# Kernel tuning notes

Measured on AMD Instinct MI355X. Metric: run time of the kernel, lower is better.

Reference implementation:

```python
import jax, jax.numpy as jnp
import numpy as np

HS = 512; L = 4; T = 128; M = 2048; FF = 2048; NH = 4; DH = HS // NH
STDV = 1.0 / float(np.sqrt(HS))


def setup_inputs() -> dict:
    key = jax.random.key(0)
    ks = iter(jax.random.split(key, 32))

    def u(shape):
        return jax.random.uniform(next(ks), shape, jnp.float32, -STDV, STDV)

    return {
        "x": jax.random.normal(next(ks), (1, T, HS), jnp.float32),
        "historical_states": jax.random.normal(next(ks), (M, L, HS), jnp.float32),
        "Wx": u((L, 3, HS, HS)), "bx": u((L, 3, HS)),
        "Wh": u((L, 3, HS, HS)), "bh": u((L, 3, HS)),
        "sa_Win": u((L, 3 * HS, HS)), "sa_bin": u((L, 3 * HS)),
        "sa_Wo": u((L, HS, HS)), "sa_bo": u((L, HS)),
        "ca_Win": u((L, 3 * HS, HS)), "ca_bin": u((L, 3 * HS)),
        "ca_Wo": u((L, HS, HS)), "ca_bo": u((L, HS)),
        "ff_W1": u((L, FF, HS)), "ff_b1": u((L, FF)),
        "ff_W2": u((L, HS, FF)), "ff_b2": u((L, HS)),
        "ln_g": u((L, 3, HS)), "ln_b": u((L, 3, HS)),
    }


def _layer_norm(v, g, b):
    m = v.mean(-1, keepdims=True)
    var = ((v - m) ** 2).mean(-1, keepdims=True)
    return (v - m) / jnp.sqrt(var + 1e-5) * g + b


def _forward(x, historical_states, Wx, bx, Wh, bh, sa_Win, sa_bin, sa_Wo, sa_bo,
             ca_Win, ca_bin, ca_Wo, ca_bo, ff_W1, ff_b1, ff_W2, ff_b2, ln_g, ln_b):
    n_layers, _, hs, _ = Wx.shape
    # Cross-attn K/V over the static historical memory are time-invariant: precompute once.
    Wk = ca_Win[:, hs:2 * hs, :]; bk = ca_bin[:, hs:2 * hs]
    Wv = ca_Win[:, 2 * hs:, :]; bv = ca_bin[:, 2 * hs:]
    K = (jnp.einsum('mle,lfe->lmf', historical_states, Wk) + bk[:, None, :]).reshape(n_layers, -1, NH, DH)
    V = (jnp.einsum('mle,lfe->lmf', historical_states, Wv) + bv[:, None, :]).reshape(n_layers, -1, NH, DH)
    scale = 1.0 / jnp.sqrt(jnp.asarray(DH, x.dtype))

    def decoder(i, f):
        # post-norm TransformerDecoderLayer, tgt length 1, eval mode (no dropout).
        # Self-attn over a single position: softmax of one logit == 1 -> out = Wo @ (Wv_self f + bv_self) + bo.
        v_sa = sa_Win[i, 2 * hs:] @ f + sa_bin[i, 2 * hs:]
        sa = sa_Wo[i] @ v_sa + sa_bo[i]
        x1 = _layer_norm(f + sa, ln_g[i, 0], ln_b[i, 0])
        q = (ca_Win[i, :hs] @ x1 + ca_bin[i, :hs]).reshape(NH, DH)
        att = jax.nn.softmax(jnp.einsum('hd,mhd->hm', q, K[i]) * scale, axis=-1)
        ctx = jnp.einsum('hm,mhd->hd', att, V[i]).reshape(hs)
        x2 = _layer_norm(x1 + ca_Wo[i] @ ctx + ca_bo[i], ln_g[i, 1], ln_b[i, 1])
        ff = ff_W2[i] @ jax.nn.relu(ff_W1[i] @ x2 + ff_b1[i]) + ff_b2[i]
        return _layer_norm(x2 + ff, ln_g[i, 2], ln_b[i, 2])

    def step(carry, x_t):
        h_prev, c_prev = carry  # (L, HS) each; batch is structurally 1
        xin = x_t
        h_new = []; c_new = []
        for i in range(n_layers):
            z = (jnp.einsum('gij,j->gi', Wx[i], xin) + bx[i]
                 + jnp.einsum('gij,j->gi', Wh[i], h_prev[i]) + bh[i])  # (3, HS)
            i_t = jax.nn.sigmoid(z[0]); f0 = jax.nn.sigmoid(z[1]); g_t = jnp.tanh(z[2])
            f_t = jax.nn.sigmoid(c_prev[i] - decoder(i, f0))
            c_i = f_t * c_prev[i] + i_t * g_t
            xin = jnp.tanh(c_i)
            h_new.append(xin); c_new.append(c_i)
        h = jnp.stack(h_new); c = jnp.stack(c_new)
        return (h, c), h[-1]

    h0 = jnp.zeros((n_layers, hs), x.dtype)
    c0 = jnp.zeros((n_layers, hs), x.dtype)
    (h_T, c_T), hidden = jax.lax.scan(step, (h0, c0), x[0])  # hidden: (T, HS)
    return hidden[None], h_T[:, None, :], c_T[:, None, :]


def reference(x, historical_states, Wx, bx, Wh, bh, sa_Win, sa_bin, sa_Wo, sa_bo,
              ca_Win, ca_bin, ca_Wo, ca_bo, ff_W1, ff_b1, ff_W2, ff_b2, ln_g, ln_b):
    return _forward(x, historical_states, Wx, bx, Wh, bh, sa_Win, sa_bin, sa_Wo, sa_bo,
                    ca_Win, ca_bin, ca_Wo, ca_bo, ff_W1, ff_b1, ff_W2, ff_b2, ln_g, ln_b)
```

## Files before the change

### kernel.cpp

```cpp
#include <hip/hip_runtime.h>

#define HS   512
#define LNUM 4
#define TT   128
#define MMEM 2048
#define FFD  2048
#define NB   256
#define NT   512
#define INV512 (1.0f/512.0f)
#define QSCALE 0.08838834764831845f

constexpr size_t KHALF = (size_t)LNUM*MMEM*HS/2;
constexpr size_t HHALF = (size_t)LNUM*HS*HS/2;
constexpr size_t FHALF = (size_t)LNUM*FFD*HS/2;
constexpr size_t OFF_KBF    = 0;
constexpr size_t OFF_VBF    = OFF_KBF    + KHALF;
constexpr size_t OFF_WCOMBBF= OFF_VBF    + KHALF;
constexpr size_t OFF_WQTBF  = OFF_WCOMBBF+ HHALF;
constexpr size_t OFF_W2TBF  = OFF_WQTBF  + HHALF;
constexpr size_t OFF_FFW1BF = OFF_W2TBF  + FHALF;
constexpr size_t OFF_CAWOBF = OFF_FFW1BF + FHALF;
constexpr size_t OFF_CSA    = OFF_CAWOBF + HHALF;
constexpr size_t OFF_SQ     = OFF_CSA    + (size_t)LNUM*HS;
constexpr size_t OFF_CBQ    = OFF_SQ     + (size_t)LNUM*HS;
constexpr size_t OFF_STATE = OFF_CBQ   + (size_t)LNUM*HS;
constexpr size_t OFF_H     = OFF_STATE;
constexpr size_t OFF_C     = OFF_H     + 2*LNUM*HS;
constexpr size_t OFF_XING  = OFF_C     + 2*LNUM*HS;
constexpr size_t OFF_Z1    = OFF_XING  + HS;
constexpr size_t OFF_Z02   = OFF_Z1    + HS;
constexpr size_t OFF_T2G   = OFF_Z02   + 2*HS;
constexpr size_t OFF_YP    = OFF_T2G   + HS;
constexpr size_t OFF_Y2P   = OFF_YP    + 4*HS;
constexpr size_t OFF_CTXP  = OFF_Y2P   + 8*HS;
constexpr size_t OFF_DENS  = OFF_CTXP  + 8*HS;
constexpr size_t OFF_S1S   = OFF_DENS  + 128;
constexpr size_t OFF_S2S   = OFF_S1S   + 64;
constexpr size_t OFF_J1    = OFF_S2S   + 64;
constexpr size_t OFF_J2    = OFF_J1    + 65*32;
constexpr size_t OFF_FLAGS = OFF_J2    + 128*32;
constexpr size_t WS_TOTAL  = OFF_FLAGS + (size_t)NB*32;

__device__ __forceinline__ float wred(float v) {
#pragma unroll
  for (int m = 32; m; m >>= 1) v += __shfl_xor(v, m);
  return v;
}
__device__ __forceinline__ float sigm(float x) { return 1.0f/(1.0f+__expf(-x)); }

__device__ __forceinline__ unsigned short f2bf(float f) {
  unsigned u = __float_as_uint(f);
  unsigned r = (u + 0x7fffu + ((u >> 16) & 1u)) >> 16;
  return (unsigned short)r;
}
__device__ __forceinline__ float bf2f(unsigned short h) {
  return __uint_as_float(((unsigned)h) << 16);
}

__device__ __forceinline__ float ald(const float* p) {
  return __hip_atomic_load(p, __ATOMIC_RELAXED, __HIP_MEMORY_SCOPE_AGENT);
}
__device__ __forceinline__ void ast(float* p, float v) {
  __hip_atomic_store(p, v, __ATOMIC_RELAXED, __HIP_MEMORY_SCOPE_AGENT);
}
__device__ __forceinline__ unsigned aldu(const unsigned* p) {
  return __hip_atomic_load(p, __ATOMIC_RELAXED, __HIP_MEMORY_SCOPE_AGENT);
}
__device__ __forceinline__ void astu(unsigned* p, unsigned v) {
  __hip_atomic_store(p, v, __ATOMIC_RELAXED, __HIP_MEMORY_SCOPE_AGENT);
}

template <class F>
__device__ __forceinline__ void barrier_pf(unsigned* flags, unsigned g, F&& pf) {
  asm volatile("s_waitcnt vmcnt(0)" ::: "memory");
  __syncthreads();
  if (threadIdx.x == 0) astu(flags + (size_t)blockIdx.x*32, g);
  pf();
  if (threadIdx.x < NB) {
    const unsigned* f = flags + (size_t)threadIdx.x*32;
    while ((int)(aldu(f) - g) < 0) __builtin_amdgcn_s_sleep(2);
  }
  __syncthreads();
}

__device__ __forceinline__ void jflag(unsigned* J, int id, unsigned val) {
  asm volatile("s_waitcnt vmcnt(0)" ::: "memory");
  __syncthreads();
  if (threadIdx.x == 0) astu(J + (size_t)id*32, val);
}
template <class F>
__device__ __forceinline__ void jwait_pf(unsigned* J, int n, unsigned val, F&& pf) {
  pf();
  if (threadIdx.x < n) {
    const unsigned* f = J + (size_t)threadIdx.x*32;
    while ((int)(aldu(f) - val) < 0) __builtin_amdgcn_s_sleep(1);
  }
  __syncthreads();
}

__device__ __forceinline__ void slotred32(const float* slots, float* sh, int o,
                                          int w, int lane) {
  if (w == 0) {
    float a = (lane < 32) ? ald(slots + lane*2) : ald(slots + (lane-32)*2 + 1);
#pragma unroll
    for (int m = 16; m; m >>= 1) a += __shfl_xor(a, m);
    if (lane == 0)  sh[o]   = a;
    if (lane == 32) sh[o+1] = a;
  }
}


__global__ __launch_bounds__(256) void kv_gemm(
    const float* __restrict__ hist, const float* __restrict__ caWin,
    const float* __restrict__ caBin, unsigned short* __restrict__ out, int koff) {
  __shared__ float As[16][64];
  __shared__ float Bs[16][64];
  const int l = blockIdx.z, m0 = blockIdx.x*64, f0 = blockIdx.y*64;
  const int tid = threadIdx.x, tm = tid >> 4, tf = tid & 15;
  float acc[4][4] = {};
  for (int e0 = 0; e0 < HS; e0 += 16) {
#pragma unroll
    for (int it = 0; it < 4; ++it) {
      int idx = tid + it*256, k = idx & 15, mm = idx >> 4;
      As[k][mm] = hist[((size_t)(m0+mm)*LNUM + l)*HS + e0 + k];
      Bs[k][mm] = caWin[((size_t)l*(3*HS) + koff + f0 + mm)*HS + e0 + k];
    }
    __syncthreads();
#pragma unroll
    for (int k = 0; k < 16; ++k) {
      float a[4], b[4];
#pragma unroll
      for (int x = 0; x < 4; ++x) { a[x] = As[k][tm*4+x]; b[x] = Bs[k][tf*4+x]; }
#pragma unroll
      for (int x = 0; x < 4; ++x)
#pragma unroll
        for (int y = 0; y < 4; ++y) acc[x][y] += a[x]*b[y];
    }
    __syncthreads();
  }
#pragma unroll
  for (int x = 0; x < 4; ++x)
#pragma unroll
    for (int y = 0; y < 4; ++y) {
      int m = m0 + tm*4 + x, f = f0 + tf*4 + y;
      out[((size_t)l*MMEM + m)*HS + f] = f2bf(acc[x][y] + caBin[l*(3*HS) + koff + f]);
    }
}

__global__ __launch_bounds__(256) void wcomb_gemm(
    const float* __restrict__ saWo, const float* __restrict__ saWin,
    unsigned short* __restrict__ wcomb) {
  __shared__ float As[16][64];
  __shared__ float Bs[16][64];
  const int l = blockIdx.z, f0 = blockIdx.x*64, j0 = blockIdx.y*64;
  const int tid = threadIdx.x, tm = tid >> 4, tf = tid & 15;
  float acc[4][4] = {};
  for (int e0 = 0; e0 < HS; e0 += 16) {
#pragma unroll
    for (int it = 0; it < 4; ++it) {
      int idx = tid + it*256;
      { int k = idx & 15, ff = idx >> 4;
        As[k][ff] = saWo[((size_t)l*HS + f0+ff)*HS + e0 + k]; }
      { int jj = idx & 63, k = idx >> 6;
        Bs[k][jj] = saWin[((size_t)l*(3*HS) + 2*HS + e0 + k)*HS + j0 + jj]; }
    }
    __syncthreads();
#pragma unroll
    for (int k = 0; k < 16; ++k) {
      float a[4], b[4];
#pragma unroll
      for (int x = 0; x < 4; ++x) { a[x] = As[k][tm*4+x]; b[x] = Bs[k][tf*4+x]; }
#pragma unroll
      for (int x = 0; x < 4; ++x)
#pragma unroll
        for (int y = 0; y < 4; ++y) acc[x][y] += a[x]*b[y];
    }
    __syncthreads();
  }
#pragma unroll
  for (int x = 0; x < 4; ++x)
#pragma unroll
    for (int y = 0; y < 4; ++y)
      wcomb[(size_t)l*HS*HS + (size_t)(f0+tm*4+x)*HS + (j0+tf*4+y)] = f2bf(acc[x][y]);
}

__global__ __launch_bounds__(256) void transpose_scale_bf(
    const float* __restrict__ in, size_t inLS, int R, int C,
    const float* __restrict__ g, size_t gLS,
    unsigned short* __restrict__ out, size_t outLS) {
  __shared__ float tile[32][33];
  const int l = blockIdx.z, e0 = blockIdx.x*32, f0 = blockIdx.y*32;
  const int tx = threadIdx.x & 31, ty = threadIdx.x >> 5;
#pragma unroll
  for (int r = 0; r < 32; r += 8)
    tile[ty+r][tx] = in[(size_t)l*inLS + (size_t)(f0+ty+r)*C + e0 + tx];
  __syncthreads();
#pragma unroll
  for (int r = 0; r < 32; r += 8) {
    int e = e0 + ty + r, f = f0 + tx;
    float s = g ? g[(size_t)l*gLS + e] : 1.0f;
    out[(size_t)l*outLS + (size_t)e*R + f] = f2bf(tile[tx][ty+r] * s);
  }
}

__global__ __launch_bounds__(256) void bf16_copy(
    const float* __restrict__ in, unsigned short* __restrict__ out, size_t n) {
  for (size_t i = (size_t)blockIdx.x*256 + threadIdx.x; i < n; i += (size_t)gridDim.x*256)
    out[i] = f2bf(in[i]);
}

__global__ __launch_bounds__(256) void csa_kernel(
    const float* __restrict__ saWo, const float* __restrict__ sabin,
    const float* __restrict__ sabo, float* __restrict__ csa) {
  const int w = threadIdx.x >> 6, lane = threadIdx.x & 63;
  const int row = blockIdx.x*4 + w;
  const int l = row >> 9, f = row & 511;
  float acc = 0;
#pragma unroll
  for (int k = 0; k < 8; ++k) {
    int e = lane + 64*k;
    acc += saWo[((size_t)l*HS + f)*HS + e] * sabin[l*(3*HS) + 2*HS + e];
  }
  acc = wred(acc);
  if (lane == 0) csa[row] = acc + sabo[l*HS + f];
}

__global__ __launch_bounds__(256) void sqcbq_kernel(
    const float* __restrict__ caWin, const float* __restrict__ caBin,
    const float* __restrict__ lnG, const float* __restrict__ lnB,
    float* __restrict__ sq, float* __restrict__ cbq) {
  const int w = threadIdx.x >> 6, lane = threadIdx.x & 63;
  const int row = blockIdx.x*4 + w;
  const int l = row >> 9, f = row & 511;
  float a1 = 0, a2 = 0;
#pragma unroll
  for (int k = 0; k < 8; ++k) {
    int e = lane + 64*k;
    float wv = caWin[((size_t)l*(3*HS) + f)*HS + e];
    a1 += wv * lnG[l*(3*HS) + e];
    a2 += wv * lnB[l*(3*HS) + e];
  }
  a1 = wred(a1); a2 = wred(a2);
  if (lane == 0) { sq[row] = a1; cbq[row] = a2 + caBin[l*(3*HS) + f]; }
}


__global__ __launch_bounds__(NT, 2) void seq_kernel(
    const float* __restrict__ x,
    const float* __restrict__ Wx,  const float* __restrict__ bx,
    const float* __restrict__ Wh,  const float* __restrict__ bh,
    const float* __restrict__ caBo,
    const float* __restrict__ ffB1,
    const float* __restrict__ ffB2,
    const float* __restrict__ lnG,  const float* __restrict__ lnB,
    float* __restrict__ ws, float* __restrict__ out) {
  const unsigned short* Kb    = (const unsigned short*)(ws + OFF_KBF);
  const unsigned short* Vb    = (const unsigned short*)(ws + OFF_VBF);
  const unsigned short* Wcomb = (const unsigned short*)(ws + OFF_WCOMBBF);
  const unsigned short* WqT   = (const unsigned short*)(ws + OFF_WQTBF);
  const unsigned short* W2T   = (const unsigned short*)(ws + OFF_W2TBF);
  const unsigned short* F1b   = (const unsigned short*)(ws + OFF_FFW1BF);
  const unsigned short* CaWob = (const unsigned short*)(ws + OFF_CAWOBF);
  const float* csag  = ws + OFF_CSA;
  const float* sqg   = ws + OFF_SQ;
  const float* cbqg  = ws + OFF_CBQ;
  float* hG    = ws + OFF_H;
  float* cG    = ws + OFF_C;
  float* xing  = ws + OFF_XING;
  float* z1g   = ws + OFF_Z1;
  float* z02g  = ws + OFF_Z02;
  float* t2g   = ws + OFF_T2G;
  float* Yp    = ws + OFF_YP;
  float* Y2p   = ws + OFF_Y2P;
  float* ctxP  = ws + OFF_CTXP;
  float* denS  = ws + OFF_DENS;
  float* s1s   = ws + OFF_S1S;
  float* s2s   = ws + OFF_S2S;
  unsigned* J1     = (unsigned*)(ws + OFF_J1);
  unsigned* J2     = (unsigned*)(ws + OFF_J2);
  unsigned* bflags = (unsigned*)(ws + OFF_FLAGS);

  __shared__ float sh_xin[HS], sh_h[HS], sh_vec[HS], sh_aux[HS];
  __shared__ float sh_q[128], sh_p[64], sh_t1[16];
  __shared__ float sh_red[24], sh_den[4];

  const int bid = blockIdx.x, tid = threadIdx.x;
  const int w = tid >> 6, lane = tid & 63;
  unsigned gen = 1;

  float pZx[8], pZh[8];
  float pZx2[8], pZh2[8];
  unsigned short pWc[2][8], pWq[16];
  unsigned short pK[8][2], pV[16];
  unsigned short pCa[2][8];
  unsigned short pF1[8], pW2[8];

  auto pfH1 = [&](int l) {
    if (bid < 64) {
      const float* wxr = Wx + (((size_t)l*3 + 1)*HS + bid*8 + w)*HS;
      const float* whr = Wh + (((size_t)l*3 + 1)*HS + bid*8 + w)*HS;
#pragma unroll
      for (int k = 0; k < 8; ++k) { pZx[k] = wxr[lane+64*k]; pZh[k] = whr[lane+64*k]; }
    }
  };
  auto pfH2 = [&](int l) {
    if (bid < 32) {
#pragma unroll
      for (int rr = 0; rr < 2; ++rr) {
        const unsigned short* wr = Wcomb + ((size_t)l*HS + bid*16 + w*2 + rr)*HS;
#pragma unroll
        for (int k = 0; k < 8; ++k) pWc[rr][k] = wr[lane+64*k];
      }
#pragma unroll
      for (int r = 0; r < 16; ++r)
        pWq[r] = WqT[((size_t)l*HS + bid*16 + r)*HS + tid];
    }
  };
  auto pfH3 = [&](int l) {
    if (bid >= 32 && bid < 160) {
      const int b2 = bid - 32, h = b2 >> 5, mseg = b2 & 31;
#pragma unroll
      for (int rr = 0; rr < 8; ++rr) {
        const unsigned short* kr = Kb + ((size_t)l*MMEM + mseg*64 + w*8 + rr)*HS + h*128;
        pK[rr][0] = kr[lane]; pK[rr][1] = kr[lane+64];
      }
#pragma unroll
      for (int ml = 0; ml < 16; ++ml)
        pV[ml] = Vb[((size_t)l*MMEM + mseg*64 + (tid>>7)*16 + ml)*HS + h*128 + (tid & 127)];
    }
  };
  auto pfZ = [&](int l) {
    if (bid < 32 || bid >= 160) {
      const int zb = (bid < 32) ? bid : bid - 128;
      const int rowid = zb*8 + w;
      const int g = (rowid < 512) ? 0 : 2;
      const int f = rowid & 511;
      const float* wxr = Wx + (((size_t)l*3 + g)*HS + f)*HS;
      const float* whr = Wh + (((size_t)l*3 + g)*HS + f)*HS;
#pragma unroll
      for (int k = 0; k < 8; ++k) { pZx2[k] = wxr[lane+64*k]; pZh2[k] = whr[lane+64*k]; }
    }
  };
  auto pfH4 = [&](int l) {
    if (bid < 32) {
#pragma unroll
      for (int rr = 0; rr < 2; ++rr) {
        const unsigned short* wr = CaWob + ((size_t)l*HS + bid*16 + w*2 + rr)*HS;
#pragma unroll
        for (int k = 0; k < 8; ++k) pCa[rr][k] = wr[lane+64*k];
      }
    }
  };
  auto pfH5 = [&](int l) {
    const unsigned short* wr = F1b + ((size_t)l*FFD + bid*8 + w)*HS;
#pragma unroll
    for (int k = 0; k < 8; ++k) pF1[k] = wr[lane+64*k];
#pragma unroll
    for (int r = 0; r < 8; ++r)
      pW2[r] = W2T[((size_t)l*FFD + bid*8 + r)*HS + tid];
  };

  auto do_update = [&](int ip, int parp, float& xn, float& cn) {
    const int j = tid;
    float t2v = ald(t2g + j);
    float z0  = ald(z02g + j);
    float z2  = ald(z02g + HS + j);
    float y2 = 0;
#pragma unroll
    for (int p = 0; p < 8; ++p) y2 += ald(Y2p + (size_t)p*HS + j);
    slotred32(s2s, sh_red, 16, w, lane);
    __syncthreads();
    float m2 = sh_red[16]*INV512;
    float r2 = rsqrtf(sh_red[17]*INV512 - m2*m2 + 1e-5f);
    float x2 = (t2v-m2)*r2*lnG[(ip*3+1)*HS+j] + lnB[(ip*3+1)*HS+j];
    float t3 = x2 + y2 + ffB2[ip*HS + j];
    float s_ = t3, q_ = t3*t3;
#pragma unroll
    for (int m = 32; m; m >>= 1) { s_ += __shfl_xor(s_, m); q_ += __shfl_xor(q_, m); }
    if (lane == 0) { sh_red[w] = s_; sh_red[8+w] = q_; }
    __syncthreads();
    if (tid == 0) {
      float a = 0, b = 0;
#pragma unroll
      for (int k = 0; k < 8; ++k) { a += sh_red[k]; b += sh_red[8+k]; }
      sh_red[0] = a; sh_red[1] = b;
    }
    __syncthreads();
    float m3 = sh_red[0]*INV512;
    float r3 = rsqrtf(sh_red[1]*INV512 - m3*m3 + 1e-5f);
    float d  = (t3-m3)*r3*lnG[(ip*3+2)*HS+j] + lnB[(ip*3+2)*HS+j];
    float cp = ald(cG + (parp*LNUM + ip)*HS + j);
    float ft = sigm(cp - d);
    float it = sigm(z0);
    float gt = tanhf(z2);
    cn = ft*cp + it*gt;
    xn = tanhf(cn);
  };

  pfH1(0); pfH2(0); pfH3(0);

  for (int s = 0; s < TT*LNUM; ++s) {
    const int t = s >> 2, i = s & 3;
    const int par = t & 1;
    const unsigned jv = (unsigned)(s + 1);
    if (bid < 64) {
      float xn = 0.f, cn = 0.f;
      if (s > 0) {
        const int ip = (s-1) & 3, tp = (s-1) >> 2, parp = tp & 1;
        if (bid == 0 || i > 0) {
          do_update(ip, parp, xn, cn);
          if (bid == 0) {
            ast(hG + ((parp^1)*LNUM + ip)*HS + tid, xn);
            ast(cG + ((parp^1)*LNUM + ip)*HS + tid, cn);
            if (ip == 3) out[tp*HS + tid] = xn;
          }
        }
      }
      float xv = (i == 0) ? x[t*HS + tid] : xn;
      sh_xin[tid] = xv;
      sh_h[tid]   = ald(hG + (par*LNUM + i)*HS + tid);
      if (bid == 0) ast(xing + tid, xv);
      __syncthreads();
      const int f = bid*8 + w;
      float acc = 0;
#pragma unroll
      for (int k = 0; k < 8; ++k) {
        int e = lane + 64*k;
        acc += pZx[k]*sh_xin[e] + pZh[k]*sh_h[e];
      }
      acc = wred(acc);
      if (lane == 0) ast(z1g + f, acc + bx[(i*3+1)*HS + f] + bh[(i*3+1)*HS + f]);
      jflag(J1, bid, jv);
    } else if (bid == 64) {
#pragma unroll
      for (int p = 0; p < 4; ++p) ast(Yp + (size_t)p*HS + tid, 0.f);
      jflag(J1, 64, jv);
    } else if (bid == 65) {
#pragma unroll
      for (int p = 0; p < 8; ++p) ast(ctxP + (size_t)p*HS + tid, 0.f);
    } else if (bid == 66) {
      jwait_pf(J1, 65, jv, [&]{});
#pragma unroll
      for (int p = 0; p < 8; ++p) ast(Y2p + (size_t)p*HS + tid, 0.f);
    }
    if (bid < 32) {
      jwait_pf(J1, 65, jv, [&]{});
      sh_vec[tid] = sigm(ald(z1g + tid));
      __syncthreads();
#pragma unroll
      for (int rr = 0; rr < 2; ++rr) {
        const int r = w*2 + rr, j = bid*16 + r;
        float acc = 0;
#pragma unroll
        for (int k = 0; k < 8; ++k) acc += bf2f(pWc[rr][k])*sh_vec[lane + 64*k];
        acc = wred(acc);
        if (lane == 0) {
          float t1v = sh_vec[j] + acc + csag[i*HS + j];
          sh_t1[r]  = t1v;
          sh_aux[r] = t1v;
        }
      }
      __syncthreads();
      {
        float yl = 0;
#pragma unroll
        for (int r = 0; r < 16; ++r) yl += sh_aux[r] * bf2f(pWq[r]);
        atomicAdd(&Yp[(size_t)(bid & 3)*HS + tid], yl);
      }
      if (w == 0 && lane < 16) {
        float v = sh_aux[lane], s_ = v, q_ = v*v;
#pragma unroll
        for (int m = 8; m; m >>= 1) { s_ += __shfl_xor(s_, m); q_ += __shfl_xor(q_, m); }
        if (lane == 0) { ast(s1s + bid*2, s_); ast(s1s + bid*2 + 1, q_); }
      }
    }
    barrier_pf(bflags, gen, [&]{ pfZ(i); pfH4(i); pfH5(i); });
    if (bid >= 32 && bid < 160) {
      const int b2 = bid - 32, h = b2 >> 5, mseg = b2 & 31;
      slotred32(s1s, sh_red, 18, w, lane);
      __syncthreads();
      if (tid < 128) {
        float m1 = sh_red[18]*INV512;
        float r1 = rsqrtf(sh_red[19]*INV512 - m1*m1 + 1e-5f);
        int f = h*128 + tid;
        float Ysum = 0;
#pragma unroll
        for (int p = 0; p < 4; ++p) Ysum += ald(Yp + (size_t)p*HS + f);
        sh_q[tid] = r1*(Ysum - m1*sqg[i*HS + f]) + cbqg[i*HS + f];
      }
      __syncthreads();
#pragma unroll
      for (int rr = 0; rr < 8; ++rr) {
        float acc = sh_q[lane]*bf2f(pK[rr][0]) + sh_q[lane+64]*bf2f(pK[rr][1]);
        acc = wred(acc);
        if (lane == 0) sh_p[w*8 + rr] = __expf(acc * QSCALE);
      }
      __syncthreads();
      {
        const int d = tid & 127, mg = tid >> 7;
        float acc = 0;
#pragma unroll
        for (int ml = 0; ml < 16; ++ml) acc += sh_p[mg*16 + ml] * bf2f(pV[ml]);
        atomicAdd(&ctxP[(size_t)((b2 & 1)*4 + mg)*HS + h*128 + d], acc);
      }
      if (w == 0) {
        float v = wred(sh_p[lane]);
        if (lane == 0) ast(denS + h*32 + mseg, v);
      }
      jflag(J2, b2, jv);
    } else {
      const int zb = (bid < 32) ? bid : bid - 128;
      if (bid >= 160) {
        sh_xin[tid] = ald(xing + tid);
        sh_h[tid]   = ald(hG + (par*LNUM + i)*HS + tid);
      }
      __syncthreads();
      const int rowid = zb*8 + w;
      const int g = (rowid < 512) ? 0 : 2;
      const int f = rowid & 511;
      float acc = 0;
#pragma unroll
      for (int k = 0; k < 8; ++k) {
        int e = lane + 64*k;
        acc += pZx2[k]*sh_xin[e] + pZh2[k]*sh_h[e];
      }
      acc = wred(acc);
      if (lane == 0) ast(z02g + (g ? HS : 0) + f, acc + bx[(i*3+g)*HS + f] + bh[(i*3+g)*HS + f]);
      if (bid < 32) {
        jwait_pf(J2, 128, jv, [&]{});
        slotred32(s1s, sh_red, 18, w, lane);
        if (w >= 4) {
          float v = (lane < 32) ? ald(denS + (w-4)*32 + lane) : 0.f;
#pragma unroll
          for (int m = 16; m; m >>= 1) v += __shfl_xor(v, m);
          if (lane == 0) sh_den[w-4] = v;
        }
        __syncthreads();
        const float m1 = sh_red[18]*INV512;
        const float r1 = rsqrtf(sh_red[19]*INV512 - m1*m1 + 1e-5f);
        {
          float c = 0;
#pragma unroll
          for (int p = 0; p < 8; ++p) c += ald(ctxP + (size_t)p*HS + tid);
          sh_vec[tid] = c / sh_den[tid >> 7];
        }
        __syncthreads();
#pragma unroll
        for (int rr = 0; rr < 2; ++rr) {
          const int r = w*2 + rr, j = bid*16 + r;
          float a2 = 0;
#pragma unroll
          for (int k = 0; k < 8; ++k) a2 += bf2f(pCa[rr][k])*sh_vec[lane + 64*k];
          a2 = wred(a2);
          if (lane == 0) {
            float x1 = (sh_t1[r]-m1)*r1*lnG[(i*3)*HS + j] + lnB[(i*3)*HS + j];
            float t2v = x1 + a2 + caBo[i*HS + j];
            ast(t2g + j, t2v);
            sh_aux[r] = t2v;
          }
        }
        __syncthreads();
        if (w == 0 && lane < 16) {
          float v = sh_aux[lane], s_ = v, q_ = v*v;
#pragma unroll
          for (int m = 8; m; m >>= 1) { s_ += __shfl_xor(s_, m); q_ += __shfl_xor(q_, m); }
          if (lane == 0) { ast(s2s + bid*2, s_); ast(s2s + bid*2 + 1, q_); }
        }
      }
    }
    barrier_pf(bflags, gen+1, [&]{ const int nl = (s+1) & 3; pfH1(nl); pfH2(nl); pfH3(nl); });
    {
      slotred32(s2s, sh_red, 16, w, lane);
      __syncthreads();
      const float m2 = sh_red[16]*INV512;
      const float r2 = rsqrtf(sh_red[17]*INV512 - m2*m2 + 1e-5f);
      sh_vec[tid] = (ald(t2g + tid)-m2)*r2*lnG[(i*3+1)*HS + tid] + lnB[(i*3+1)*HS + tid];
      __syncthreads();
      const int kk = bid*8 + w;
      float acc = 0;
#pragma unroll
      for (int k = 0; k < 8; ++k) acc += bf2f(pF1[k])*sh_vec[lane + 64*k];
      acc = wred(acc);
      if (lane == 0) sh_aux[w] = fmaxf(acc + ffB1[i*FFD + kk], 0.f);
      __syncthreads();
      float yl = 0;
#pragma unroll
      for (int r = 0; r < 8; ++r) yl += sh_aux[r] * bf2f(pW2[r]);
      atomicAdd(&Y2p[(size_t)(bid & 7)*HS + tid], yl);
    }
    barrier_pf(bflags, gen+2, [&]{});
    gen += 3;
  }

  if (bid == 0) {
    float xn, cn;
    do_update(3, 1, xn, cn);
    out[127*HS + tid] = xn;
    out[TT*HS + 3*HS + tid] = xn;
    out[TT*HS + LNUM*HS + 3*HS + tid] = cn;
#pragma unroll
    for (int ii = 0; ii < 3; ++ii) {
      out[TT*HS + ii*HS + tid]            = ald(hG + (0*LNUM + ii)*HS + tid);
      out[TT*HS + LNUM*HS + ii*HS + tid]  = ald(cG + (0*LNUM + ii)*HS + tid);
    }
  }
}

extern "C" void kernel_launch(void* const* d_in, const int* in_sizes, int n_in,
                              void* d_out, int out_size, void* d_ws, size_t ws_size,
                              hipStream_t stream) {
  const float* x      = (const float*)d_in[0];
  const float* hist   = (const float*)d_in[1];
  const float* Wx     = (const float*)d_in[2];
  const float* bx     = (const float*)d_in[3];
  const float* Wh     = (const float*)d_in[4];
  const float* bh     = (const float*)d_in[5];
  const float* saWin  = (const float*)d_in[6];
  const float* saBin  = (const float*)d_in[7];
  const float* saWo   = (const float*)d_in[8];
  const float* saBo   = (const float*)d_in[9];
  const float* caWin  = (const float*)d_in[10];
  const float* caBin  = (const float*)d_in[11];
  const float* caWo   = (const float*)d_in[12];
  const float* caBo   = (const float*)d_in[13];
  const float* ffW1   = (const float*)d_in[14];
  const float* ffB1   = (const float*)d_in[15];
  const float* ffW2   = (const float*)d_in[16];
  const float* ffB2   = (const float*)d_in[17];
  const float* lnG    = (const float*)d_in[18];
  const float* lnB    = (const float*)d_in[19];
  float* ws  = (float*)d_ws;
  float* out = (float*)d_out;

  hipMemsetAsync((char*)d_ws + OFF_STATE*sizeof(float), 0,
                 (WS_TOTAL - OFF_STATE)*sizeof(float), stream);

  kv_gemm<<<dim3(MMEM/64, HS/64, LNUM), 256, 0, stream>>>(
      hist, caWin, caBin, (unsigned short*)(ws + OFF_KBF), HS);
  kv_gemm<<<dim3(MMEM/64, HS/64, LNUM), 256, 0, stream>>>(
      hist, caWin, caBin, (unsigned short*)(ws + OFF_VBF), 2*HS);
  wcomb_gemm<<<dim3(HS/64, HS/64, LNUM), 256, 0, stream>>>(
      saWo, saWin, (unsigned short*)(ws + OFF_WCOMBBF));
  csa_kernel<<<(LNUM*HS)/4, 256, 0, stream>>>(saWo, saBin, saBo, ws + OFF_CSA);
  transpose_scale_bf<<<dim3(HS/32, HS/32, LNUM), 256, 0, stream>>>(
      caWin, (size_t)(3*HS)*HS, HS, HS, lnG, (size_t)(3*HS),
      (unsigned short*)(ws + OFF_WQTBF), (size_t)HS*HS);
  sqcbq_kernel<<<(LNUM*HS)/4, 256, 0, stream>>>(caWin, caBin, lnG, lnB, ws + OFF_SQ, ws + OFF_CBQ);
  transpose_scale_bf<<<dim3(FFD/32, HS/32, LNUM), 256, 0, stream>>>(
      ffW2, (size_t)HS*FFD, HS, FFD, nullptr, 0,
      (unsigned short*)(ws + OFF_W2TBF), (size_t)FFD*HS);
  bf16_copy<<<2048, 256, 0, stream>>>(ffW1, (unsigned short*)(ws + OFF_FFW1BF),
                                      (size_t)LNUM*FFD*HS);
  bf16_copy<<<1024, 256, 0, stream>>>(caWo, (unsigned short*)(ws + OFF_CAWOBF),
                                      (size_t)LNUM*HS*HS);

  seq_kernel<<<NB, NT, 0, stream>>>(x, Wx, bx, Wh, bh, caBo,
                                    ffB1, ffB2, lnG, lnB, ws, out);
}
```

Baseline: 13.82 ms.

## Repack prefetched weights into contiguous per-thread blocks for vectorized 128-bit loads

Reorganizes the preprocessed weight buffers (Wq, W2 packed per block/thread, V stored transposed, K and other rows read as 8 contiguous elements per lane) so each thread's register prefetch becomes one or two uint4/float4 loads instead of many scalar 16-bit/32-bit loads. The dot-product loops are rewritten to unpack bf16 pairs from 32-bit words, and the K scoring now uses 16-lane sub-reductions. Launch bounds for the persistent kernel drop from 2 to 1 blocks per SM, allowing more registers. This targets the instruction and memory-transaction overhead of the per-step weight prefetch, at the cost of uncoalesced strided writes in the packing kernels and transposed V stores.

```diff
diff --git a/kernel.cpp b/kernel.cpp
--- a/kernel.cpp
+++ b/kernel.cpp
@@ -10,15 +10,17 @@
 #define INV512 (1.0f/512.0f)
 #define QSCALE 0.08838834764831845f
 
+typedef unsigned short ushortt;
+
 constexpr size_t KHALF = (size_t)LNUM*MMEM*HS/2;
 constexpr size_t HHALF = (size_t)LNUM*HS*HS/2;
 constexpr size_t FHALF = (size_t)LNUM*FFD*HS/2;
 constexpr size_t OFF_KBF    = 0;
 constexpr size_t OFF_VBF    = OFF_KBF    + KHALF;
 constexpr size_t OFF_WCOMBBF= OFF_VBF    + KHALF;
-constexpr size_t OFF_WQTBF  = OFF_WCOMBBF+ HHALF;
-constexpr size_t OFF_W2TBF  = OFF_WQTBF  + HHALF;
-constexpr size_t OFF_FFW1BF = OFF_W2TBF  + FHALF;
+constexpr size_t OFF_WQP    = OFF_WCOMBBF+ HHALF;
+constexpr size_t OFF_W2P    = OFF_WQP    + HHALF;
+constexpr size_t OFF_FFW1BF = OFF_W2P    + FHALF;
 constexpr size_t OFF_CAWOBF = OFF_FFW1BF + FHALF;
 constexpr size_t OFF_CSA    = OFF_CAWOBF + HHALF;
 constexpr size_t OFF_SQ     = OFF_CSA    + (size_t)LNUM*HS;
@@ -47,14 +49,19 @@
   return v;
 }
 __device__ __forceinline__ float sigm(float x) { return 1.0f/(1.0f+__expf(-x)); }
-
-__device__ __forceinline__ unsigned short f2bf(float f) {
+__device__ __forceinline__ ushortt f2bf(float f) {
   unsigned u = __float_as_uint(f);
-  unsigned r = (u + 0x7fffu + ((u >> 16) & 1u)) >> 16;
-  return (unsigned short)r;
-}
-__device__ __forceinline__ float bf2f(unsigned short h) {
-  return __uint_as_float(((unsigned)h) << 16);
+  return (ushortt)((u + 0x7fffu + ((u >> 16) & 1u)) >> 16);
+}
+__device__ __forceinline__ float bflo(unsigned v){ return __uint_as_float(v << 16); }
+__device__ __forceinline__ float bfhi(unsigned v){ return __uint_as_float(v & 0xffff0000u); }
+__device__ __forceinline__ void ld8bfp(const ushortt* p, unsigned* d) {
+  uint4 v = *(const uint4*)p;
+  d[0] = v.x; d[1] = v.y; d[2] = v.z; d[3] = v.w;
+}
+__device__ __forceinline__ void ld8f(const float* p, float* d) {
+  float4 a = *(const float4*)p, b = *(const float4*)(p + 4);
+  d[0]=a.x; d[1]=a.y; d[2]=a.z; d[3]=a.w; d[4]=b.x; d[5]=b.y; d[6]=b.z; d[7]=b.w;
 }
 
 __device__ __forceinline__ float ald(const float* p) {
@@ -82,7 +89,6 @@
   }
   __syncthreads();
 }
-
 __device__ __forceinline__ void jflag(unsigned* J, int id, unsigned val) {
   asm volatile("s_waitcnt vmcnt(0)" ::: "memory");
   __syncthreads();
@@ -97,7 +103,6 @@
   }
   __syncthreads();
 }
-
 __device__ __forceinline__ void slotred32(const float* slots, float* sh, int o,
                                           int w, int lane) {
   if (w == 0) {
@@ -112,7 +117,7 @@
 
 __global__ __launch_bounds__(256) void kv_gemm(
     const float* __restrict__ hist, const float* __restrict__ caWin,
-    const float* __restrict__ caBin, unsigned short* __restrict__ out, int koff) {
+    const float* __restrict__ caBin, ushortt* __restrict__ out, int koff, int vt) {
   __shared__ float As[16][64];
   __shared__ float Bs[16][64];
   const int l = blockIdx.z, m0 = blockIdx.x*64, f0 = blockIdx.y*64;
@@ -130,26 +135,28 @@
     for (int k = 0; k < 16; ++k) {
       float a[4], b[4];
 #pragma unroll
-      for (int x = 0; x < 4; ++x) { a[x] = As[k][tm*4+x]; b[x] = Bs[k][tf*4+x]; }
-#pragma unroll
-      for (int x = 0; x < 4; ++x)
-#pragma unroll
-        for (int y = 0; y < 4; ++y) acc[x][y] += a[x]*b[y];
+      for (int xx = 0; xx < 4; ++xx) { a[xx] = As[k][tm*4+xx]; b[xx] = Bs[k][tf*4+xx]; }
+#pragma unroll
+      for (int xx = 0; xx < 4; ++xx)
+#pragma unroll
+        for (int y = 0; y < 4; ++y) acc[xx][y] += a[xx]*b[y];
     }
     __syncthreads();
   }
 #pragma unroll
-  for (int x = 0; x < 4; ++x)
+  for (int xx = 0; xx < 4; ++xx)
 #pragma unroll
     for (int y = 0; y < 4; ++y) {
-      int m = m0 + tm*4 + x, f = f0 + tf*4 + y;
-      out[((size_t)l*MMEM + m)*HS + f] = f2bf(acc[x][y] + caBin[l*(3*HS) + koff + f]);
+      int m = m0 + tm*4 + xx, f = f0 + tf*4 + y;
+      ushortt v = f2bf(acc[xx][y] + caBin[l*(3*HS) + koff + f]);
+      if (vt) out[(size_t)l*MMEM*HS + (size_t)f*MMEM + m] = v;
+      else    out[((size_t)l*MMEM + m)*HS + f] = v;
     }
 }
 
 __global__ __launch_bounds__(256) void wcomb_gemm(
     const float* __restrict__ saWo, const float* __restrict__ saWin,
-    unsigned short* __restrict__ wcomb) {
+    ushortt* __restrict__ wcomb) {
   __shared__ float As[16][64];
   __shared__ float Bs[16][64];
   const int l = blockIdx.z, f0 = blockIdx.x*64, j0 = blockIdx.y*64;
@@ -169,42 +176,44 @@
     for (int k = 0; k < 16; ++k) {
       float a[4], b[4];
 #pragma unroll
-      for (int x = 0; x < 4; ++x) { a[x] = As[k][tm*4+x]; b[x] = Bs[k][tf*4+x]; }
-#pragma unroll
-      for (int x = 0; x < 4; ++x)
-#pragma unroll
-        for (int y = 0; y < 4; ++y) acc[x][y] += a[x]*b[y];
+      for (int xx = 0; xx < 4; ++xx) { a[xx] = As[k][tm*4+xx]; b[xx] = Bs[k][tf*4+xx]; }
+#pragma unroll
+      for (int xx = 0; xx < 4; ++xx)
+#pragma unroll
+        for (int y = 0; y < 4; ++y) acc[xx][y] += a[xx]*b[y];
     }
     __syncthreads();
   }
 #pragma unroll
-  for (int x = 0; x < 4; ++x)
+  for (int xx = 0; xx < 4; ++xx)
 #pragma unroll
     for (int y = 0; y < 4; ++y)
-      wcomb[(size_t)l*HS*HS + (size_t)(f0+tm*4+x)*HS + (j0+tf*4+y)] = f2bf(acc[x][y]);
-}
-
-__global__ __launch_bounds__(256) void transpose_scale_bf(
-    const float* __restrict__ in, size_t inLS, int R, int C,
-    const float* __restrict__ g, size_t gLS,
-    unsigned short* __restrict__ out, size_t outLS) {
-  __shared__ float tile[32][33];
-  const int l = blockIdx.z, e0 = blockIdx.x*32, f0 = blockIdx.y*32;
-  const int tx = threadIdx.x & 31, ty = threadIdx.x >> 5;
-#pragma unroll
-  for (int r = 0; r < 32; r += 8)
-    tile[ty+r][tx] = in[(size_t)l*inLS + (size_t)(f0+ty+r)*C + e0 + tx];
-  __syncthreads();
-#pragma unroll
-  for (int r = 0; r < 32; r += 8) {
-    int e = e0 + ty + r, f = f0 + tx;
-    float s = g ? g[(size_t)l*gLS + e] : 1.0f;
-    out[(size_t)l*outLS + (size_t)e*R + f] = f2bf(tile[tx][ty+r] * s);
+      wcomb[(size_t)l*HS*HS + (size_t)(f0+tm*4+xx)*HS + (j0+tf*4+y)] = f2bf(acc[xx][y]);
+}
+
+__global__ __launch_bounds__(256) void pack_wq(
+    const float* __restrict__ caWin, const float* __restrict__ lnG,
+    ushortt* __restrict__ wqp) {
+  const int b = blockIdx.x, l = blockIdx.y;
+  for (int idx = threadIdx.x; idx < 512*16; idx += 256) {
+    int f = idx >> 4, r = idx & 15, j = b*16 + r;
+    wqp[(((size_t)l*32 + b)*512 + f)*16 + r] =
+        f2bf(caWin[((size_t)l*3*HS + f)*HS + j] * lnG[l*3*HS + j]);
+  }
+}
+
+__global__ __launch_bounds__(256) void pack_w2(
+    const float* __restrict__ ffW2, ushortt* __restrict__ w2p) {
+  const int bid = blockIdx.x, l = blockIdx.y;
+  for (int idx = threadIdx.x; idx < 512*8; idx += 256) {
+    int f = idx >> 3, r = idx & 7;
+    w2p[(((size_t)l*NB + bid)*512 + f)*8 + r] =
+        f2bf(ffW2[((size_t)l*HS + f)*FFD + bid*8 + r]);
   }
 }
 
 __global__ __launch_bounds__(256) void bf16_copy(
-    const float* __restrict__ in, unsigned short* __restrict__ out, size_t n) {
+    const float* __restrict__ in, ushortt* __restrict__ out, size_t n) {
   for (size_t i = (size_t)blockIdx.x*256 + threadIdx.x; i < n; i += (size_t)gridDim.x*256)
     out[i] = f2bf(in[i]);
 }
@@ -245,7 +254,7 @@
 }
 
 
-__global__ __launch_bounds__(NT, 2) void seq_kernel(
+__global__ __launch_bounds__(NT, 1) void seq_kernel(
     const float* __restrict__ x,
     const float* __restrict__ Wx,  const float* __restrict__ bx,
     const float* __restrict__ Wh,  const float* __restrict__ bh,
@@ -254,13 +263,13 @@
     const float* __restrict__ ffB2,
     const float* __restrict__ lnG,  const float* __restrict__ lnB,
     float* __restrict__ ws, float* __restrict__ out) {
-  const unsigned short* Kb    = (const unsigned short*)(ws + OFF_KBF);
-  const unsigned short* Vb    = (const unsigned short*)(ws + OFF_VBF);
-  const unsigned short* Wcomb = (const unsigned short*)(ws + OFF_WCOMBBF);
-  const unsigned short* WqT   = (const unsigned short*)(ws + OFF_WQTBF);
-  const unsigned short* W2T   = (const unsigned short*)(ws + OFF_W2TBF);
-  const unsigned short* F1b   = (const unsigned short*)(ws + OFF_FFW1BF);
-  const unsigned short* CaWob = (const unsigned short*)(ws + OFF_CAWOBF);
+  const ushortt* Kb    = (const ushortt*)(ws + OFF_KBF);
+  const ushortt* Vt    = (const ushortt*)(ws + OFF_VBF);
+  const ushortt* Wcomb = (const ushortt*)(ws + OFF_WCOMBBF);
+  const ushortt* WQP   = (const ushortt*)(ws + OFF_WQP);
+  const ushortt* W2P   = (const ushortt*)(ws + OFF_W2P);
+  const ushortt* F1b   = (const ushortt*)(ws + OFF_FFW1BF);
+  const ushortt* CaWob = (const ushortt*)(ws + OFF_CAWOBF);
   const float* csag  = ws + OFF_CSA;
   const float* sqg   = ws + OFF_SQ;
   const float* cbqg  = ws + OFF_CBQ;
@@ -288,45 +297,41 @@
   const int w = tid >> 6, lane = tid & 63;
   unsigned gen = 1;
 
-  float pZx[8], pZh[8];
-  float pZx2[8], pZh2[8];
-  unsigned short pWc[2][8], pWq[16];
-  unsigned short pK[8][2], pV[16];
-  unsigned short pCa[2][8];
-  unsigned short pF1[8], pW2[8];
+  float    pZx[8],  pZh[8];
+  float    pZx2[8], pZh2[8];
+  unsigned pWc[2][4], pWq[8];
+  unsigned pK[2][4],  pV[8];
+  unsigned pCa[2][4];
+  unsigned pF1[4], pW2[4];
 
   auto pfH1 = [&](int l) {
     if (bid < 64) {
-      const float* wxr = Wx + (((size_t)l*3 + 1)*HS + bid*8 + w)*HS;
-      const float* whr = Wh + (((size_t)l*3 + 1)*HS + bid*8 + w)*HS;
-#pragma unroll
-      for (int k = 0; k < 8; ++k) { pZx[k] = wxr[lane+64*k]; pZh[k] = whr[lane+64*k]; }
+      const size_t ro = (((size_t)l*3 + 1)*HS + bid*8 + w)*HS + lane*8;
+      ld8f(Wx + ro, pZx);
+      ld8f(Wh + ro, pZh);
     }
   };
   auto pfH2 = [&](int l) {
     if (bid < 32) {
 #pragma unroll
-      for (int rr = 0; rr < 2; ++rr) {
-        const unsigned short* wr = Wcomb + ((size_t)l*HS + bid*16 + w*2 + rr)*HS;
-#pragma unroll
-        for (int k = 0; k < 8; ++k) pWc[rr][k] = wr[lane+64*k];
-      }
-#pragma unroll
-      for (int r = 0; r < 16; ++r)
-        pWq[r] = WqT[((size_t)l*HS + bid*16 + r)*HS + tid];
+      for (int rr = 0; rr < 2; ++rr)
+        ld8bfp(Wcomb + ((size_t)l*HS + bid*16 + w*2 + rr)*HS + lane*8, pWc[rr]);
+      const ushortt* q = WQP + (((size_t)l*32 + bid)*512 + tid)*16;
+      ld8bfp(q,     pWq);
+      ld8bfp(q + 8, pWq + 4);
     }
   };
   auto pfH3 = [&](int l) {
     if (bid >= 32 && bid < 160) {
-      const int b2 = bid - 32, h = b2 >> 5, mseg = b2 & 31;
-#pragma unroll
-      for (int rr = 0; rr < 8; ++rr) {
-        const unsigned short* kr = Kb + ((size_t)l*MMEM + mseg*64 + w*8 + rr)*HS + h*128;
-        pK[rr][0] = kr[lane]; pK[rr][1] = kr[lane+64];
-      }
-#pragma unroll
-      for (int ml = 0; ml < 16; ++ml)
-        pV[ml] = Vb[((size_t)l*MMEM + mseg*64 + (tid>>7)*16 + ml)*HS + h*128 + (tid & 127)];
+      const int b2 = bid - 32, h = b2 >> 5, ms = b2 & 31;
+#pragma unroll
+      for (int rr = 0; rr < 2; ++rr)
+        ld8bfp(Kb + ((size_t)l*MMEM + ms*64 + w*8 + (lane>>4) + 4*rr)*HS
+                  + h*128 + (lane & 15)*8, pK[rr]);
+      const ushortt* vp = Vt + (size_t)l*MMEM*HS
+                        + ((size_t)h*128 + (tid & 127))*MMEM + ms*64 + (tid >> 7)*16;
+      ld8bfp(vp,     pV);
+      ld8bfp(vp + 8, pV + 4);
     }
   };
   auto pfZ = [&](int l) {
@@ -335,29 +340,21 @@
       const int rowid = zb*8 + w;
       const int g = (rowid < 512) ? 0 : 2;
       const int f = rowid & 511;
-      const float* wxr = Wx + (((size_t)l*3 + g)*HS + f)*HS;
-      const float* whr = Wh + (((size_t)l*3 + g)*HS + f)*HS;
-#pragma unroll
-      for (int k = 0; k < 8; ++k) { pZx2[k] = wxr[lane+64*k]; pZh2[k] = whr[lane+64*k]; }
+      const size_t ro = (((size_t)l*3 + g)*HS + f)*HS + lane*8;
+      ld8f(Wx + ro, pZx2);
+      ld8f(Wh + ro, pZh2);
     }
   };
   auto pfH4 = [&](int l) {
     if (bid < 32) {
 #pragma unroll
-      for (int rr = 0; rr < 2; ++rr) {
-        const unsigned short* wr = CaWob + ((size_t)l*HS + bid*16 + w*2 + rr)*HS;
-#pragma unroll
-        for (int k = 0; k < 8; ++k) pCa[rr][k] = wr[lane+64*k];
-      }
+      for (int rr = 0; rr < 2; ++rr)
+        ld8bfp(CaWob + ((size_t)l*HS + bid*16 + w*2 + rr)*HS + lane*8, pCa[rr]);
     }
   };
   auto pfH5 = [&](int l) {
-    const unsigned short* wr = F1b + ((size_t)l*FFD + bid*8 + w)*HS;
-#pragma unroll
-    for (int k = 0; k < 8; ++k) pF1[k] = wr[lane+64*k];
-#pragma unroll
-    for (int r = 0; r < 8; ++r)
-      pW2[r] = W2T[((size_t)l*FFD + bid*8 + r)*HS + tid];
+    ld8bfp(F1b + ((size_t)l*FFD + bid*8 + w)*HS + lane*8, pF1);
+    ld8bfp(W2P + (((size_t)l*NB + bid)*512 + tid)*8, pW2);
   };
 
   auto do_update = [&](int ip, int parp, float& xn, float& cn) {
@@ -366,8 +363,13 @@
     float z0  = ald(z02g + j);
     float z2  = ald(z02g + HS + j);
     float y2 = 0;
-#pragma unroll
-    for (int p = 0; p < 8; ++p) y2 += ald(Y2p + (size_t)p*HS + j);
+    {
+      float yv[8];
+#pragma unroll
+      for (int p = 0; p < 8; ++p) yv[p] = ald(Y2p + (size_t)p*HS + j);
+#pragma unroll
+      for (int p = 0; p < 8; ++p) y2 += yv[p];
+    }
     slotred32(s2s, sh_red, 16, w, lane);
     __syncthreads();
     float m2 = sh_red[16]*INV512;
@@ -424,10 +426,8 @@
       const int f = bid*8 + w;
       float acc = 0;
 #pragma unroll
-      for (int k = 0; k < 8; ++k) {
-        int e = lane + 64*k;
-        acc += pZx[k]*sh_xin[e] + pZh[k]*sh_h[e];
-      }
+      for (int m = 0; m < 8; ++m)
+        acc += pZx[m]*sh_xin[lane*8+m] + pZh[m]*sh_h[lane*8+m];
       acc = wred(acc);
       if (lane == 0) ast(z1g + f, acc + bx[(i*3+1)*HS + f] + bh[(i*3+1)*HS + f]);
       jflag(J1, bid, jv);
@@ -452,7 +452,10 @@
         const int r = w*2 + rr, j = bid*16 + r;
         float acc = 0;
 #pragma unroll
-        for (int k = 0; k < 8; ++k) acc += bf2f(pWc[rr][k])*sh_vec[lane + 64*k];
+        for (int k = 0; k < 4; ++k) {
+          unsigned pw = pWc[rr][k];
+          acc += bflo(pw)*sh_vec[lane*8 + 2*k] + bfhi(pw)*sh_vec[lane*8 + 2*k + 1];
+        }
         acc = wred(acc);
         if (lane == 0) {
           float t1v = sh_vec[j] + acc + csag[i*HS + j];
@@ -464,7 +467,10 @@
       {
         float yl = 0;
 #pragma unroll
-        for (int r = 0; r < 16; ++r) yl += sh_aux[r] * bf2f(pWq[r]);
+        for (int q = 0; q < 8; ++q) {
+          unsigned pw = pWq[q];
+          yl += sh_aux[2*q]*bflo(pw) + sh_aux[2*q+1]*bfhi(pw);
+        }
         atomicAdd(&Yp[(size_t)(bid & 3)*HS + tid], yl);
       }
       if (w == 0 && lane < 16) {
@@ -476,7 +482,7 @@
     }
     barrier_pf(bflags, gen, [&]{ pfZ(i); pfH4(i); pfH5(i); });
     if (bid >= 32 && bid < 160) {
-      const int b2 = bid - 32, h = b2 >> 5, mseg = b2 & 31;
+      const int b2 = bid - 32, h = b2 >> 5;
       slotred32(s1s, sh_red, 18, w, lane);
       __syncthreads();
       if (tid < 128) {
@@ -490,22 +496,31 @@
       }
       __syncthreads();
 #pragma unroll
-      for (int rr = 0; rr < 8; ++rr) {
-        float acc = sh_q[lane]*bf2f(pK[rr][0]) + sh_q[lane+64]*bf2f(pK[rr][1]);
-        acc = wred(acc);
-        if (lane == 0) sh_p[w*8 + rr] = __expf(acc * QSCALE);
+      for (int rr = 0; rr < 2; ++rr) {
+        float sc = 0;
+#pragma unroll
+        for (int k = 0; k < 4; ++k) {
+          unsigned pw = pK[rr][k];
+          sc += bflo(pw)*sh_q[(lane & 15)*8 + 2*k] + bfhi(pw)*sh_q[(lane & 15)*8 + 2*k + 1];
+        }
+#pragma unroll
+        for (int msk = 8; msk; msk >>= 1) sc += __shfl_xor(sc, msk);
+        if ((lane & 15) == 0) sh_p[w*8 + (lane >> 4) + 4*rr] = __expf(sc * QSCALE);
       }
       __syncthreads();
       {
         const int d = tid & 127, mg = tid >> 7;
         float acc = 0;
 #pragma unroll
-        for (int ml = 0; ml < 16; ++ml) acc += sh_p[mg*16 + ml] * bf2f(pV[ml]);
+        for (int q = 0; q < 8; ++q) {
+          unsigned pw = pV[q];
+          acc += sh_p[mg*16 + 2*q]*bflo(pw) + sh_p[mg*16 + 2*q + 1]*bfhi(pw);
+        }
         atomicAdd(&ctxP[(size_t)((b2 & 1)*4 + mg)*HS + h*128 + d], acc);
       }
       if (w == 0) {
         float v = wred(sh_p[lane]);
-        if (lane == 0) ast(denS + h*32 + mseg, v);
+        if (lane == 0) ast(denS + h*32 + (b2 & 31), v);
       }
       jflag(J2, b2, jv);
     } else {
@@ -520,10 +535,8 @@
       const int f = rowid & 511;
       float acc = 0;
 #pragma unroll
-      for (int k = 0; k < 8; ++k) {
-        int e = lane + 64*k;
-        acc += pZx2[k]*sh_xin[e] + pZh2[k]*sh_h[e];
-      }
+      for (int m = 0; m < 8; ++m)
+        acc += pZx2[m]*sh_xin[lane*8+m] + pZh2[m]*sh_h[lane*8+m];
       acc = wred(acc);
       if (lane == 0) ast(z02g + (g ? HS : 0) + f, acc + bx[(i*3+g)*HS + f] + bh[(i*3+g)*HS + f]);
       if (bid < 32) {
@@ -550,7 +563,10 @@
           const int r = w*2 + rr, j = bid*16 + r;
           float a2 = 0;
 #pragma unroll
-          for (int k = 0; k < 8; ++k) a2 += bf2f(pCa[rr][k])*sh_vec[lane + 64*k];
+          for (int k = 0; k < 4; ++k) {
+            unsigned pw = pCa[rr][k];
+            a2 += bflo(pw)*sh_vec[lane*8 + 2*k] + bfhi(pw)*sh_vec[lane*8 + 2*k + 1];
+          }
           a2 = wred(a2);
           if (lane == 0) {
             float x1 = (sh_t1[r]-m1)*r1*lnG[(i*3)*HS + j] + lnB[(i*3)*HS + j];
@@ -579,13 +595,19 @@
       const int kk = bid*8 + w;
       float acc = 0;
 #pragma unroll
-      for (int k = 0; k < 8; ++k) acc += bf2f(pF1[k])*sh_vec[lane + 64*k];
+      for (int k = 0; k < 4; ++k) {
+        unsigned pw = pF1[k];
+        acc += bflo(pw)*sh_vec[lane*8 + 2*k] + bfhi(pw)*sh_vec[lane*8 + 2*k + 1];
+      }
       acc = wred(acc);
       if (lane == 0) sh_aux[w] = fmaxf(acc + ffB1[i*FFD + kk], 0.f);
       __syncthreads();
       float yl = 0;
 #pragma unroll
-      for (int r = 0; r < 8; ++r) yl += sh_aux[r] * bf2f(pW2[r]);
+      for (int q = 0; q < 4; ++q) {
+        unsigned pw = pW2[q];
+        yl += sh_aux[2*q]*bflo(pw) + sh_aux[2*q+1]*bfhi(pw);
+      }
       atomicAdd(&Y2p[(size_t)(bid & 7)*HS + tid], yl);
     }
     barrier_pf(bflags, gen+2, [&]{});
@@ -636,23 +658,17 @@
                  (WS_TOTAL - OFF_STATE)*sizeof(float), stream);
 
   kv_gemm<<<dim3(MMEM/64, HS/64, LNUM), 256, 0, stream>>>(
-      hist, caWin, caBin, (unsigned short*)(ws + OFF_KBF), HS);
+      hist, caWin, caBin, (ushortt*)(ws + OFF_KBF), HS, 0);
   kv_gemm<<<dim3(MMEM/64, HS/64, LNUM), 256, 0, stream>>>(
-      hist, caWin, caBin, (unsigned short*)(ws + OFF_VBF), 2*HS);
+      hist, caWin, caBin, (ushortt*)(ws + OFF_VBF), 2*HS, 1);
   wcomb_gemm<<<dim3(HS/64, HS/64, LNUM), 256, 0, stream>>>(
-      saWo, saWin, (unsigned short*)(ws + OFF_WCOMBBF));
+      saWo, saWin, (ushortt*)(ws + OFF_WCOMBBF));
   csa_kernel<<<(LNUM*HS)/4, 256, 0, stream>>>(saWo, saBin, saBo, ws + OFF_CSA);
-  transpose_scale_bf<<<dim3(HS/32, HS/32, LNUM), 256, 0, stream>>>(
-      caWin, (size_t)(3*HS)*HS, HS, HS, lnG, (size_t)(3*HS),
-      (unsigned short*)(ws + OFF_WQTBF), (size_t)HS*HS);
+  pack_wq<<<dim3(32, LNUM), 256, 0, stream>>>(caWin, lnG, (ushortt*)(ws + OFF_WQP));
   sqcbq_kernel<<<(LNUM*HS)/4, 256, 0, stream>>>(caWin, caBin, lnG, lnB, ws + OFF_SQ, ws + OFF_CBQ);
-  transpose_scale_bf<<<dim3(FFD/32, HS/32, LNUM), 256, 0, stream>>>(
-      ffW2, (size_t)HS*FFD, HS, FFD, nullptr, 0,
-      (unsigned short*)(ws + OFF_W2TBF), (size_t)FFD*HS);
-  bf16_copy<<<2048, 256, 0, stream>>>(ffW1, (unsigned short*)(ws + OFF_FFW1BF),
-                                      (size_t)LNUM*FFD*HS);
-  bf16_copy<<<1024, 256, 0, stream>>>(caWo, (unsigned short*)(ws + OFF_CAWOBF),
-                                      (size_t)LNUM*HS*HS);
+  pack_w2<<<dim3(NB, LNUM), 256, 0, stream>>>(ffW2, (ushortt*)(ws + OFF_W2P));
+  bf16_copy<<<2048, 256, 0, stream>>>(ffW1, (ushortt*)(ws + OFF_FFW1BF), (size_t)LNUM*FFD*HS);
+  bf16_copy<<<1024, 256, 0, stream>>>(caWo, (ushortt*)(ws + OFF_CAWOBF), (size_t)LNUM*HS*HS);
 
   seq_kernel<<<NB, NT, 0, stream>>>(x, Wx, bx, Wh, bh, caBo,
                                     ffB1, ffB2, lnG, lnB, ws, out);
```

Result: faster. 11.09 ms (-19.8%).
